# Kernel tuning notes

Measured on AMD Instinct MI355X. Metric: run time of the kernel, lower is better.

Reference implementation:

```python
import jax, jax.numpy as jnp
import numpy as np

K, D = 1024, 256
B, H, W = 16, 64, 64


def setup_inputs() -> dict:
    key = jax.random.key(0)
    k1, k2 = jax.random.split(key)
    z_e_x = jax.random.normal(k1, (B, D, H, W), dtype=jnp.float32)
    # nn.Embedding weight initialized uniform(-1/K, 1/K)
    embedding = jax.random.uniform(k2, (K, D), dtype=jnp.float32,
                                   minval=-1.0 / K, maxval=1.0 / K)
    return {"z_e_x": z_e_x, "embedding": embedding}


def reference(z_e_x, embedding):
    # permute(0,2,3,1): [B,D,H,W] -> [B,H,W,D]
    z = jnp.transpose(z_e_x, (0, 2, 3, 1))
    flat = z.reshape(-1, z.shape[-1])  # [N, D], N = B*H*W
    # squared L2 distances: ||z||^2 - 2 z.e + ||e||^2  -> [N, K]
    dists = (jnp.sum(flat * flat, axis=1, keepdims=True)
             - 2.0 * flat @ embedding.T
             + jnp.sum(embedding * embedding, axis=1))
    indices = jnp.argmin(dists, axis=1)  # [N]
    # vq() returns latents with the spatial shape [B, H, W]
    return indices.reshape(z.shape[:-1]).astype(jnp.int32)
```

## Files before the change

kernel.cpp:

```cpp
#include <hip/hip_runtime.h>


#define D_DIM  256
#define K_DIM  1024
#define HW     4096
#define N_TOT  65536
#define NSPLIT 4
#define NKT    4
#define KT     64
#define KSPL   (K_DIM / NSPLIT)
#define F32MAX 3.402823466e38f


__global__ void ee_kernel(const float* __restrict__ e, float* __restrict__ ee) {
#pragma clang fp contract(off)
    int k = blockIdx.x * blockDim.x + threadIdx.x;
    if (k >= K_DIM) return;
    const float* row = e + (size_t)k * D_DIM;
    float total = 0.0f;
    #pragma unroll
    for (int h = 0; h < 2; ++h) {
        const float* a = row + h * 128;
        float r[8];
        #pragma unroll
        for (int j = 0; j < 8; ++j) { float v = a[j]; r[j] = v * v; }
        #pragma unroll
        for (int i = 8; i < 128; i += 8) {
            #pragma unroll
            for (int j = 0; j < 8; ++j) { float v = a[i + j]; r[j] = r[j] + v * v; }
        }
        float s = ((r[0] + r[1]) + (r[2] + r[3])) + ((r[4] + r[5]) + (r[6] + r[7]));
        total = (h == 0) ? s : (total + s);
    }
    ee[k] = total;
}


__global__ void a_kernel(const float* __restrict__ z, float* __restrict__ A) {
#pragma clang fp contract(off)
    int t = blockIdx.x * blockDim.x + threadIdx.x;
    int n = t >> 1;
    int h = t & 1;
    int b  = n >> 12;
    int hw = n & (HW - 1);
    const float* base = z + (size_t)b * D_DIM * HW + hw + (size_t)(h * 128) * HW;
    float r[8];
    #pragma unroll
    for (int j = 0; j < 8; ++j) { float v = base[(size_t)j * HW]; r[j] = v * v; }
    #pragma unroll
    for (int i = 8; i < 128; i += 8) {
        #pragma unroll
        for (int j = 0; j < 8; ++j) {
            float v = base[(size_t)(i + j) * HW];
            r[j] = r[j] + v * v;
        }
    }
    float s = ((r[0] + r[1]) + (r[2] + r[3])) + ((r[4] + r[5]) + (r[6] + r[7]));
    float other = __shfl_xor(s, 1);
    if (h == 0) A[n] = s + other;
}


__global__ void et_kernel(const float* __restrict__ e, float* __restrict__ eT) {
    __shared__ float t[32][33];
    const int k0 = blockIdx.x * 32;
    const int d0 = blockIdx.y * 32;
    const int tx = threadIdx.x;
    const int ty = threadIdx.y;
    #pragma unroll
    for (int i = 0; i < 32; i += 8)
        t[ty + i][tx] = 2.0f * e[(size_t)(k0 + ty + i) * D_DIM + d0 + tx];
    __syncthreads();
    #pragma unroll
    for (int i = 0; i < 32; i += 8)
        eT[(size_t)(d0 + ty + i) * K_DIM + k0 + tx] = t[tx][ty + i];
}


__device__ __forceinline__ void kt_pass(const float* __restrict__ zp,
                                        const float* __restrict__ eT,
                                        int kbase,
                                        float (&za)[8], float (&zb)[8],
                                        float (&acc)[KT]) {
#pragma clang fp contract(off)
    #pragma unroll 1
    for (int it = 0; it < 16; ++it) {
        const int base = it * 16;
        #pragma unroll
        for (int i = 0; i < 8; ++i)
            zb[i] = zp[(size_t)((base + 8 + i) & (D_DIM - 1)) * HW];
        #pragma unroll
        for (int dd = 0; dd < 8; ++dd) {
            const float zv = za[dd];
            const float* __restrict__ er = eT + (size_t)(base + dd) * K_DIM + kbase;
            #pragma unroll
            for (int j = 0; j < KT; ++j)
                acc[j] = fmaf(zv, er[j], acc[j]);
        }
        #pragma unroll
        for (int i = 0; i < 8; ++i)
            za[i] = zp[(size_t)((base + 16 + i) & (D_DIM - 1)) * HW];
        #pragma unroll
        for (int dd = 0; dd < 8; ++dd) {
            const float zv = zb[dd];
            const float* __restrict__ er = eT + (size_t)(base + 8 + dd) * K_DIM + kbase;
            #pragma unroll
            for (int j = 0; j < KT; ++j)
                acc[j] = fmaf(zv, er[j], acc[j]);
        }
    }
}


__launch_bounds__(256, 4)
__global__ void vq_partial(const float* __restrict__ z, const float* __restrict__ eT,
                           const float* __restrict__ A, const float* __restrict__ ee,
                           unsigned long long* __restrict__ packed) {
#pragma clang fp contract(off)
    const int tid  = threadIdx.x;
    const int s    = blockIdx.x & (NSPLIT - 1);
    const int slab = blockIdx.x >> 2;
    const int n    = slab * 256 + tid;
    const int b    = n >> 12;
    const int hw   = n & (HW - 1);
    const float* __restrict__ zp = z + (size_t)b * D_DIM * HW + hw;
    const int kb0 = s * KSPL;

    const float An = A[n];
    float bestv = F32MAX;
    int   bestk = 0;
    float za[8], zb[8];

    #pragma unroll
    for (int i = 0; i < 8; ++i) za[i] = zp[(size_t)i * HW];

    #pragma unroll 1
    for (int kt = 0; kt < NKT; ++kt) {
        const int kbase = kb0 + kt * KT;
        float acc[KT];
        #pragma unroll
        for (int j = 0; j < KT; ++j) acc[j] = 0.0f;
        kt_pass(zp, eT, kbase, za, zb, acc);
        #pragma unroll
        for (int j = 0; j < KT; ++j) {
            const float dist = (An - acc[j]) + ee[kbase + j];
            if (dist < bestv) { bestv = dist; bestk = kbase + j; }
        }
    }

    unsigned int vb = __float_as_uint(bestv);
    vb = (vb & 0x80000000u) ? ~vb : (vb | 0x80000000u);
    atomicMin(&packed[n], ((unsigned long long)vb << 32) | (unsigned int)bestk);
}

__global__ void unpack_kernel(const unsigned long long* __restrict__ packed,
                              int* __restrict__ out) {
    int n = blockIdx.x * blockDim.x + threadIdx.x;
    out[n] = (int)(packed[n] & 0xFFFFFFFFull);
}

extern "C" void kernel_launch(void* const* d_in, const int* in_sizes, int n_in,
                              void* d_out, int out_size, void* d_ws, size_t ws_size,
                              hipStream_t stream) {
    const float* z   = (const float*)d_in[0];
    const float* emb = (const float*)d_in[1];
    int* out = (int*)d_out;

    float* wsEE = (float*)d_ws;
    float* wsA  = wsEE + K_DIM;
    float* wsET = wsA + N_TOT;
    unsigned long long* wsPacked =
        (unsigned long long*)(wsET + (size_t)D_DIM * K_DIM);

    hipMemsetAsync(wsPacked, 0xFF, (size_t)N_TOT * sizeof(unsigned long long),
                   stream);
    et_kernel<<<dim3(K_DIM / 32, D_DIM / 32), dim3(32, 8), 0, stream>>>(emb, wsET);
    ee_kernel<<<K_DIM / 256, 256, 0, stream>>>(emb, wsEE);
    a_kernel<<<2 * N_TOT / 256, 256, 0, stream>>>(z, wsA);
    vq_partial<<<N_TOT / 256 * NSPLIT, 256, 0, stream>>>(z, wsET, wsA, wsEE,
                                                         wsPacked);
    unpack_kernel<<<N_TOT / 256, 256, 0, stream>>>(wsPacked, out);
}
```

Before: 502.7 us.

## Stage codebook tiles into LDS with double-buffered global_load_lds

The distance kernel used to read the transposed, scaled codebook straight from global memory for every FMA group. It now copies 64x64 codebook tiles into a double-buffered LDS area using the global_load_lds DMA builtin, prefetching the next tile while the current one is consumed. The FMA loop reads float4 vectors from LDS. This adds per-chunk block barriers and 32KB of LDS per block, which may limit occupancy. It also relies on the barrier waiting for the async LDS writes to finish.

Result: slower. 653.6 us (+30.0%).

```diff
diff --git a/kernel.cpp b/kernel.cpp
--- a/kernel.cpp
+++ b/kernel.cpp
@@ -9,6 +9,7 @@
 #define NKT    4
 #define KT     64
 #define KSPL   (K_DIM / NSPLIT)
+#define DCH    64
 #define F32MAX 3.402823466e38f
 
 
@@ -77,36 +78,50 @@
 }
 
 
-__device__ __forceinline__ void kt_pass(const float* __restrict__ zp,
-                                        const float* __restrict__ eT,
-                                        int kbase,
-                                        float (&za)[8], float (&zb)[8],
-                                        float (&acc)[KT]) {
-#pragma clang fp contract(off)
-    #pragma unroll 1
-    for (int it = 0; it < 16; ++it) {
-        const int base = it * 16;
-        #pragma unroll
-        for (int i = 0; i < 8; ++i)
-            zb[i] = zp[(size_t)((base + 8 + i) & (D_DIM - 1)) * HW];
-        #pragma unroll
-        for (int dd = 0; dd < 8; ++dd) {
-            const float zv = za[dd];
-            const float* __restrict__ er = eT + (size_t)(base + dd) * K_DIM + kbase;
-            #pragma unroll
-            for (int j = 0; j < KT; ++j)
-                acc[j] = fmaf(zv, er[j], acc[j]);
-        }
-        #pragma unroll
-        for (int i = 0; i < 8; ++i)
-            za[i] = zp[(size_t)((base + 16 + i) & (D_DIM - 1)) * HW];
-        #pragma unroll
-        for (int dd = 0; dd < 8; ++dd) {
-            const float zv = zb[dd];
-            const float* __restrict__ er = eT + (size_t)(base + 8 + dd) * K_DIM + kbase;
-            #pragma unroll
-            for (int j = 0; j < KT; ++j)
-                acc[j] = fmaf(zv, er[j], acc[j]);
+__device__ __forceinline__ void stage_issue(const float* __restrict__ eT,
+                                            float* cb, int kbase, int d0, int t) {
+    #pragma unroll
+    for (int o = 0; o < 4; ++o) {
+        const float* g = eT + (size_t)(d0 + o * 16 + (t >> 4)) * K_DIM
+                       + kbase + (t & 15) * 4;
+        float* l = cb + o * 1024 + (t >> 6) * 256;
+        __builtin_amdgcn_global_load_lds(
+            (const __attribute__((address_space(1))) void*)g,
+            (__attribute__((address_space(3))) void*)l, 16, 0, 0);
+    }
+}
+
+
+__device__ __forceinline__ void zpf(const float* __restrict__ zp, int df,
+                                    float (&dst)[8]) {
+    #pragma unroll
+    for (int i = 0; i < 8; ++i)
+        dst[i] = zp[(size_t)((df + i) & (D_DIM - 1)) * HW];
+}
+
+
+__device__ __forceinline__ void fma8(const float* cb, int rb,
+                                     const float (&zr)[8], float (&acc)[KT]) {
+#pragma clang fp contract(off)
+    #pragma unroll
+    for (int dd = 0; dd < 8; ++dd) {
+        const float zv = zr[dd];
+        const float4* er = (const float4*)(cb + (size_t)(rb + dd) * KT);
+        #pragma unroll
+        for (int q = 0; q < 4; ++q) {
+            float4 e0 = er[q * 4 + 0];
+            float4 e1 = er[q * 4 + 1];
+            float4 e2 = er[q * 4 + 2];
+            float4 e3 = er[q * 4 + 3];
+            float* a = &acc[q * 16];
+            a[0]  = fmaf(zv, e0.x, a[0]);  a[1]  = fmaf(zv, e0.y, a[1]);
+            a[2]  = fmaf(zv, e0.z, a[2]);  a[3]  = fmaf(zv, e0.w, a[3]);
+            a[4]  = fmaf(zv, e1.x, a[4]);  a[5]  = fmaf(zv, e1.y, a[5]);
+            a[6]  = fmaf(zv, e1.z, a[6]);  a[7]  = fmaf(zv, e1.w, a[7]);
+            a[8]  = fmaf(zv, e2.x, a[8]);  a[9]  = fmaf(zv, e2.y, a[9]);
+            a[10] = fmaf(zv, e2.z, a[10]); a[11] = fmaf(zv, e2.w, a[11]);
+            a[12] = fmaf(zv, e3.x, a[12]); a[13] = fmaf(zv, e3.y, a[13]);
+            a[14] = fmaf(zv, e3.z, a[14]); a[15] = fmaf(zv, e3.w, a[15]);
         }
     }
 }
@@ -117,22 +132,25 @@
                            const float* __restrict__ A, const float* __restrict__ ee,
                            unsigned long long* __restrict__ packed) {
 #pragma clang fp contract(off)
-    const int tid  = threadIdx.x;
+    __shared__ __align__(16) float cbuf[2][DCH * KT];
+
+    const int t    = threadIdx.x;
     const int s    = blockIdx.x & (NSPLIT - 1);
     const int slab = blockIdx.x >> 2;
-    const int n    = slab * 256 + tid;
+    const int n    = slab * 256 + t;
     const int b    = n >> 12;
     const int hw   = n & (HW - 1);
     const float* __restrict__ zp = z + (size_t)b * D_DIM * HW + hw;
     const int kb0 = s * KSPL;
 
+    stage_issue(eT, cbuf[0], kb0, 0, t);
+    float za[8], zb[8];
+    zpf(zp, 0, za);
     const float An = A[n];
+    __syncthreads();
+
     float bestv = F32MAX;
     int   bestk = 0;
-    float za[8], zb[8];
-
-    #pragma unroll
-    for (int i = 0; i < 8; ++i) za[i] = zp[(size_t)i * HW];
 
     #pragma unroll 1
     for (int kt = 0; kt < NKT; ++kt) {
@@ -140,7 +158,28 @@
         float acc[KT];
         #pragma unroll
         for (int j = 0; j < KT; ++j) acc[j] = 0.0f;
-        kt_pass(zp, eT, kbase, za, zb, acc);
+
+        #pragma unroll 1
+        for (int ch = 0; ch < 4; ++ch) {
+            const int st = kt * 4 + ch;
+            if (st + 1 < NKT * 4) {
+                const int nst = st + 1;
+                stage_issue(eT, cbuf[nst & 1],
+                            kb0 + (nst >> 2) * KT, (nst & 3) * DCH, t);
+            }
+            const float* cb = cbuf[st & 1];
+            #pragma unroll 1
+            for (int it2 = 0; it2 < 4; ++it2) {
+                const int dg = ch * DCH + it2 * 16;
+                const int rb = it2 * 16;
+                zpf(zp, dg + 8, zb);
+                fma8(cb, rb, za, acc);
+                zpf(zp, dg + 16, za);
+                fma8(cb, rb + 8, zb, acc);
+            }
+            __syncthreads();
+        }
+
         #pragma unroll
         for (int j = 0; j < KT; ++j) {
             const float dist = (An - acc[j]) + ee[kbase + j];
```

## Remap VQ search so each wave owns 8 points with lanes over codes

Applied to the files above, without the earlier changes.

The three prep kernels (transpose, row norms, point norms) are merged into one launch. The main kernel is remapped so each wavefront handles 8 consecutive points, with its 64 lanes covering 64 codebook entries per tile. The z values become wave-uniform broadcast loads and the full K range is scanned in one kernel, finishing with a shuffle-based argmin. This drops the memset, the 64-bit atomics and the unpack kernel, and lowers register pressure so occupancy can be higher. The trade-off is that each point now sweeps the whole codebook serially per wave, and arithmetic intensity per thread is lower (8 accumulators instead of 64).

Result: slower. 743.3 us (+47.9%).

```diff
diff --git a/kernel.cpp b/kernel.cpp
--- a/kernel.cpp
+++ b/kernel.cpp
@@ -5,158 +5,140 @@
 #define K_DIM  1024
 #define HW     4096
 #define N_TOT  65536
-#define NSPLIT 4
-#define NKT    4
-#define KT     64
-#define KSPL   (K_DIM / NSPLIT)
+#define NW     8
 #define F32MAX 3.402823466e38f
 
 
-__global__ void ee_kernel(const float* __restrict__ e, float* __restrict__ ee) {
+__global__ void prep_kernel(const float* __restrict__ z, const float* __restrict__ e,
+                            float* __restrict__ eT, float* __restrict__ A,
+                            float* __restrict__ ee) {
 #pragma clang fp contract(off)
-    int k = blockIdx.x * blockDim.x + threadIdx.x;
-    if (k >= K_DIM) return;
-    const float* row = e + (size_t)k * D_DIM;
-    float total = 0.0f;
-    #pragma unroll
-    for (int h = 0; h < 2; ++h) {
-        const float* a = row + h * 128;
+    const int bid = blockIdx.x;
+    const int t   = threadIdx.x;
+
+    if (bid < 256) {
+        __shared__ float tl[32][33];
+        const int k0 = (bid & 31) * 32;
+        const int d0 = (bid >> 5) * 32;
+        const int tx = t & 31;
+        const int ty = t >> 5;
+        #pragma unroll
+        for (int i = 0; i < 32; i += 8)
+            tl[ty + i][tx] = 2.0f * e[(size_t)(k0 + ty + i) * D_DIM + d0 + tx];
+        __syncthreads();
+        #pragma unroll
+        for (int i = 0; i < 32; i += 8)
+            eT[(size_t)(d0 + ty + i) * K_DIM + k0 + tx] = tl[tx][ty + i];
+    } else if (bid < 768) {
+        const int tt = (bid - 256) * 256 + t;
+        const int n  = tt >> 1;
+        const int h  = tt & 1;
+        const int b  = n >> 12;
+        const int hw = n & (HW - 1);
+        const float* base = z + (size_t)b * D_DIM * HW + hw + (size_t)(h * 128) * HW;
         float r[8];
         #pragma unroll
-        for (int j = 0; j < 8; ++j) { float v = a[j]; r[j] = v * v; }
+        for (int j = 0; j < 8; ++j) { float v = base[(size_t)j * HW]; r[j] = v * v; }
         #pragma unroll
         for (int i = 8; i < 128; i += 8) {
             #pragma unroll
-            for (int j = 0; j < 8; ++j) { float v = a[i + j]; r[j] = r[j] + v * v; }
+            for (int j = 0; j < 8; ++j) {
+                float v = base[(size_t)(i + j) * HW];
+                r[j] = r[j] + v * v;
+            }
         }
         float s = ((r[0] + r[1]) + (r[2] + r[3])) + ((r[4] + r[5]) + (r[6] + r[7]));
-        total = (h == 0) ? s : (total + s);
-    }
-    ee[k] = total;
-}
-
-
-__global__ void a_kernel(const float* __restrict__ z, float* __restrict__ A) {
-#pragma clang fp contract(off)
-    int t = blockIdx.x * blockDim.x + threadIdx.x;
-    int n = t >> 1;
-    int h = t & 1;
-    int b  = n >> 12;
-    int hw = n & (HW - 1);
-    const float* base = z + (size_t)b * D_DIM * HW + hw + (size_t)(h * 128) * HW;
-    float r[8];
-    #pragma unroll
-    for (int j = 0; j < 8; ++j) { float v = base[(size_t)j * HW]; r[j] = v * v; }
-    #pragma unroll
-    for (int i = 8; i < 128; i += 8) {
+        float other = __shfl_xor(s, 1);
+        if (h == 0) A[n] = s + other;
+    } else {
+        const int k = (bid - 768) * 256 + t;
+        const float* row = e + (size_t)k * D_DIM;
+        float total = 0.0f;
         #pragma unroll
-        for (int j = 0; j < 8; ++j) {
-            float v = base[(size_t)(i + j) * HW];
-            r[j] = r[j] + v * v;
+        for (int h = 0; h < 2; ++h) {
+            const float* a = row + h * 128;
+            float r[8];
+            #pragma unroll
+            for (int j = 0; j < 8; ++j) { float v = a[j]; r[j] = v * v; }
+            #pragma unroll
+            for (int i = 8; i < 128; i += 8) {
+                #pragma unroll
+                for (int j = 0; j < 8; ++j) { float v = a[i + j]; r[j] = r[j] + v * v; }
+            }
+            float s = ((r[0] + r[1]) + (r[2] + r[3])) + ((r[4] + r[5]) + (r[6] + r[7]));
+            total = (h == 0) ? s : (total + s);
         }
-    }
-    float s = ((r[0] + r[1]) + (r[2] + r[3])) + ((r[4] + r[5]) + (r[6] + r[7]));
-    float other = __shfl_xor(s, 1);
-    if (h == 0) A[n] = s + other;
-}
-
-
-__global__ void et_kernel(const float* __restrict__ e, float* __restrict__ eT) {
-    __shared__ float t[32][33];
-    const int k0 = blockIdx.x * 32;
-    const int d0 = blockIdx.y * 32;
-    const int tx = threadIdx.x;
-    const int ty = threadIdx.y;
-    #pragma unroll
-    for (int i = 0; i < 32; i += 8)
-        t[ty + i][tx] = 2.0f * e[(size_t)(k0 + ty + i) * D_DIM + d0 + tx];
-    __syncthreads();
-    #pragma unroll
-    for (int i = 0; i < 32; i += 8)
-        eT[(size_t)(d0 + ty + i) * K_DIM + k0 + tx] = t[tx][ty + i];
-}
-
-
-__device__ __forceinline__ void kt_pass(const float* __restrict__ zp,
-                                        const float* __restrict__ eT,
-                                        int kbase,
-                                        float (&za)[8], float (&zb)[8],
-                                        float (&acc)[KT]) {
-#pragma clang fp contract(off)
-    #pragma unroll 1
-    for (int it = 0; it < 16; ++it) {
-        const int base = it * 16;
-        #pragma unroll
-        for (int i = 0; i < 8; ++i)
-            zb[i] = zp[(size_t)((base + 8 + i) & (D_DIM - 1)) * HW];
-        #pragma unroll
-        for (int dd = 0; dd < 8; ++dd) {
-            const float zv = za[dd];
-            const float* __restrict__ er = eT + (size_t)(base + dd) * K_DIM + kbase;
-            #pragma unroll
-            for (int j = 0; j < KT; ++j)
-                acc[j] = fmaf(zv, er[j], acc[j]);
-        }
-        #pragma unroll
-        for (int i = 0; i < 8; ++i)
-            za[i] = zp[(size_t)((base + 16 + i) & (D_DIM - 1)) * HW];
-        #pragma unroll
-        for (int dd = 0; dd < 8; ++dd) {
-            const float zv = zb[dd];
-            const float* __restrict__ er = eT + (size_t)(base + 8 + dd) * K_DIM + kbase;
-            #pragma unroll
-            for (int j = 0; j < KT; ++j)
-                acc[j] = fmaf(zv, er[j], acc[j]);
-        }
+        ee[k] = total;
     }
 }
 
 
-__launch_bounds__(256, 4)
-__global__ void vq_partial(const float* __restrict__ z, const float* __restrict__ eT,
-                           const float* __restrict__ A, const float* __restrict__ ee,
-                           unsigned long long* __restrict__ packed) {
+__launch_bounds__(256, 8)
+__global__ void vq_kernel(const float* __restrict__ z, const float* __restrict__ eT,
+                          const float* __restrict__ A, const float* __restrict__ ee,
+                          int* __restrict__ out) {
 #pragma clang fp contract(off)
-    const int tid  = threadIdx.x;
-    const int s    = blockIdx.x & (NSPLIT - 1);
-    const int slab = blockIdx.x >> 2;
-    const int n    = slab * 256 + tid;
-    const int b    = n >> 12;
-    const int hw   = n & (HW - 1);
-    const float* __restrict__ zp = z + (size_t)b * D_DIM * HW + hw;
-    const int kb0 = s * KSPL;
+    const int lane = threadIdx.x & 63;
+    const int wid  = __builtin_amdgcn_readfirstlane(threadIdx.x >> 6);
+    const int gw   = blockIdx.x * 4 + wid;
+    const int n0   = gw * NW;
+    const int b    = n0 >> 12;
+    const int hw0  = n0 & (HW - 1);
+    const float* __restrict__ zrow = z + (size_t)b * D_DIM * HW + hw0;
 
-    const float An = A[n];
-    float bestv = F32MAX;
-    int   bestk = 0;
-    float za[8], zb[8];
+    float An[NW];
+    #pragma unroll
+    for (int i = 0; i < NW; ++i) An[i] = A[n0 + i];
 
+    unsigned int bkey[NW], bk[NW];
     #pragma unroll
-    for (int i = 0; i < 8; ++i) za[i] = zp[(size_t)i * HW];
+    for (int i = 0; i < NW; ++i) { bkey[i] = 0xFFFFFFFFu; bk[i] = 0u; }
 
     #pragma unroll 1
-    for (int kt = 0; kt < NKT; ++kt) {
-        const int kbase = kb0 + kt * KT;
-        float acc[KT];
+    for (int kt = 0; kt < 16; ++kt) {
+        const int kb = kt * 64;
+        const float* __restrict__ ep = eT + kb + lane;
+
+        float acc[NW];
         #pragma unroll
-        for (int j = 0; j < KT; ++j) acc[j] = 0.0f;
-        kt_pass(zp, eT, kbase, za, zb, acc);
+        for (int i = 0; i < NW; ++i) acc[i] = 0.0f;
+
+        #pragma unroll 1
+        for (int d = 0; d < D_DIM; d += 8) {
+            float er[8];
+            #pragma unroll
+            for (int r = 0; r < 8; ++r)
+                er[r] = ep[(size_t)(d + r) * K_DIM];
+            #pragma unroll
+            for (int r = 0; r < 8; ++r) {
+                const float* zr = zrow + (size_t)(d + r) * HW;
+                #pragma unroll
+                for (int i = 0; i < NW; ++i)
+                    acc[i] = fmaf(zr[i], er[r], acc[i]);
+            }
+        }
+
+        const float eev = ee[kb + lane];
         #pragma unroll
-        for (int j = 0; j < KT; ++j) {
-            const float dist = (An - acc[j]) + ee[kbase + j];
-            if (dist < bestv) { bestv = dist; bestk = kbase + j; }
+        for (int i = 0; i < NW; ++i) {
+            const float dist = (An[i] - acc[i]) + eev;
+            unsigned int kb32 = __float_as_uint(dist);
+            kb32 ^= (unsigned int)((int)kb32 >> 31) | 0x80000000u;
+            if (kb32 < bkey[i]) { bkey[i] = kb32; bk[i] = (unsigned int)(kb + lane); }
         }
     }
 
-    unsigned int vb = __float_as_uint(bestv);
-    vb = (vb & 0x80000000u) ? ~vb : (vb | 0x80000000u);
-    atomicMin(&packed[n], ((unsigned long long)vb << 32) | (unsigned int)bestk);
-}
-
-__global__ void unpack_kernel(const unsigned long long* __restrict__ packed,
-                              int* __restrict__ out) {
-    int n = blockIdx.x * blockDim.x + threadIdx.x;
-    out[n] = (int)(packed[n] & 0xFFFFFFFFull);
+    #pragma unroll
+    for (int i = 0; i < NW; ++i) {
+        unsigned long long key =
+            ((unsigned long long)bkey[i] << 32) | (unsigned long long)bk[i];
+        #pragma unroll
+        for (int m = 1; m < 64; m <<= 1) {
+            unsigned long long o = __shfl_xor(key, m, 64);
+            if (o < key) key = o;
+        }
+        if (lane == 0) out[n0 + i] = (int)(key & 0xFFFFFFFFull);
+    }
 }
 
 extern "C" void kernel_launch(void* const* d_in, const int* in_sizes, int n_in,
@@ -169,15 +151,7 @@
     float* wsEE = (float*)d_ws;
     float* wsA  = wsEE + K_DIM;
     float* wsET = wsA + N_TOT;
-    unsigned long long* wsPacked =
-        (unsigned long long*)(wsET + (size_t)D_DIM * K_DIM);
 
-    hipMemsetAsync(wsPacked, 0xFF, (size_t)N_TOT * sizeof(unsigned long long),
-                   stream);
-    et_kernel<<<dim3(K_DIM / 32, D_DIM / 32), dim3(32, 8), 0, stream>>>(emb, wsET);
-    ee_kernel<<<K_DIM / 256, 256, 0, stream>>>(emb, wsEE);
-    a_kernel<<<2 * N_TOT / 256, 256, 0, stream>>>(z, wsA);
-    vq_partial<<<N_TOT / 256 * NSPLIT, 256, 0, stream>>>(z, wsET, wsA, wsEE,
-                                                         wsPacked);
-    unpack_kernel<<<N_TOT / 256, 256, 0, stream>>>(wsPacked, out);
+    prep_kernel<<<772, 256, 0, stream>>>(z, emb, wsET, wsA, wsEE);
+    vq_kernel<<<N_TOT / NW / 4, 256, 0, stream>>>(z, wsET, wsA, wsEE, out);
 }
```
